# Kernel tuning notes

Measured on AMD Instinct MI355X. Metric: run time of the kernel, lower is better.

The kernel has to match this reference:

```python
import jax, jax.numpy as jnp
import numpy as np

B, C, W, H, HEADS = 32, 512, 32, 32, 8
D = C // HEADS
N = W * H
LN_EPS = 1e-5


def setup_inputs() -> dict:
    key = jax.random.key(0)
    ks = jax.random.split(key, 11)
    s = 1.0 / np.sqrt(C)
    return {
        "x": jax.random.normal(ks[0], (B, C, W, H), jnp.float32),
        "Wq": jax.random.normal(ks[1], (C, C), jnp.float32) * s,
        "bq": jax.random.normal(ks[2], (C,), jnp.float32) * 0.01,
        "Wk": jax.random.normal(ks[3], (C, C), jnp.float32) * s,
        "bk": jax.random.normal(ks[4], (C,), jnp.float32) * 0.01,
        "Wv": jax.random.normal(ks[5], (C, C), jnp.float32) * s,
        "bv": jax.random.normal(ks[6], (C,), jnp.float32) * 0.01,
        "rel_h": jax.random.normal(ks[7], (1, HEADS, D, 1, H), jnp.float32),
        "rel_w": jax.random.normal(ks[8], (1, HEADS, D, W, 1), jnp.float32),
        "ln_w": jnp.ones((C, W, H), jnp.float32),
        "ln_b": jnp.zeros((C, W, H), jnp.float32),
    }


def reference(x, Wq, bq, Wk, bk, Wv, bv, rel_h, rel_w, ln_w, ln_b):
    b, c, w, h = x.shape
    nh, d, n = HEADS, c // HEADS, w * h

    def proj(Wm, bm):
        # 1x1 conv == per-pixel linear: out[b,o,w,h] = sum_c Wm[o,c] x[b,c,w,h] + bm[o]
        y = jnp.einsum('bcwh,oc->bowh', x, Wm) + bm[None, :, None, None]
        return y.reshape(b, nh, d, n)

    q = proj(Wq, bq)  # [B,h,d,N]
    k = proj(Wk, bk)
    v = proj(Wv, bv)

    # content-content: q^T k -> [B,h,N,N]
    cc = jnp.einsum('bhdn,bhdm->bhnm', q, k)
    # content-position: (rel_h + rel_w) flattened to [h,d,N], permuted, matmul with q
    pos = (rel_h + rel_w).reshape(nh, d, n)  # [h,d,N]
    cp = jnp.einsum('hdn,bhdm->bhnm', pos, q)

    attn = jax.nn.softmax(cc + cp, axis=-1)  # [B,h,N,N]
    # out = v @ attn^T  -> [B,h,d,N]
    out = jnp.einsum('bhdn,bhmn->bhdm', v, attn)
    out = out.reshape(b, c, w, h)

    # LayerNorm over [C,W,H] with elementwise affine, then residual
    mu = jnp.mean(out, axis=(1, 2, 3), keepdims=True)
    var = jnp.var(out, axis=(1, 2, 3), keepdims=True)
    out = (out - mu) * jax.lax.rsqrt(var + LN_EPS) * ln_w[None] + ln_b[None]
    return out + x
```

## Files before the change

### kernel.cpp

```cpp
#include <hip/hip_runtime.h>
#include <stdint.h>

typedef _Float16 f16x8 __attribute__((ext_vector_type(8)));
typedef _Float16 f16x4 __attribute__((ext_vector_type(4)));
typedef __fp16   fp16x2 __attribute__((ext_vector_type(2)));
typedef float f32x4  __attribute__((ext_vector_type(4)));

__device__ __forceinline__ _Float16 f2h(float f){ return (_Float16)f; }

#define NB   32
#define NC   512
#define NH   8
#define ND   64
#define NN   1024

#define LOG2E 1.44269504f

__global__ __launch_bounds__(256) void wt_conv(const float* __restrict__ Wq,
                                               const float* __restrict__ Wk,
                                               const float* __restrict__ Wv,
                                               _Float16* __restrict__ Wt){
  int idx = blockIdx.x * 256 + threadIdx.x;
  int sel = idx >> 18;
  const float* W = (sel == 0) ? Wq : (sel == 1) ? Wk : Wv;
  Wt[idx] = f2h(W[idx & 262143]);
}

__global__ __launch_bounds__(256) void transpose_x(const float* __restrict__ x,
                                                   _Float16* __restrict__ xT){
  __shared__ float tile[32][33];
  int n0 = blockIdx.x * 32, c0 = blockIdx.y * 32, b = blockIdx.z;
  int t = threadIdx.x;
  int tn = t & 31, tc = t >> 5;
#pragma unroll
  for (int k = 0; k < 4; k++)
    tile[tc + 8*k][tn] = x[(b*NC + c0 + tc + 8*k)*NN + n0 + tn];
  __syncthreads();
#pragma unroll
  for (int k = 0; k < 4; k++)
    xT[(b*NN + n0 + tc + 8*k)*NC + c0 + tn] = f2h(tile[tn][tc + 8*k]);
}

__global__ __launch_bounds__(256) void pos_conv(const float* __restrict__ rel_h,
                                                const float* __restrict__ rel_w,
                                                _Float16* __restrict__ pos_t){
  int idx = blockIdx.x * 256 + threadIdx.x;
  int d = idx & 63, n = (idx >> 6) & 1023, h = idx >> 16;
  int ww = n >> 5, hh = n & 31;
  float v = rel_h[(h*ND + d)*32 + hh] + rel_w[(h*ND + d)*32 + ww];
  pos_t[idx] = f2h(v);
}

#define ASTR 72
#define TSTR 136

__global__ __launch_bounds__(256) void proj_gemm(const _Float16* __restrict__ Wt,
                                                 const _Float16* __restrict__ xT,
                                                 const float* __restrict__ bq,
                                                 const float* __restrict__ bk,
                                                 const float* __restrict__ bv,
                                                 _Float16* __restrict__ q_ws,
                                                 _Float16* __restrict__ k_ws,
                                                 _Float16* __restrict__ v_ws){
  __shared__ _Float16 smem[2 * 128 * ASTR];
  _Float16* As = smem;
  _Float16* Bs = smem + 128 * ASTR;

  int mt = blockIdx.x;
  int nt = blockIdx.y;
  int b  = blockIdx.z;
  int t = threadIdx.x, lane = t & 63, w = t >> 6;
  int wm = w >> 1, wn = w & 1;
  int lr = lane & 15, lg = lane >> 4;

  f32x4 acc[4][4];
#pragma unroll
  for (int i = 0; i < 4; i++)
#pragma unroll
    for (int j = 0; j < 4; j++) acc[i][j] = (f32x4)0.f;

  const _Float16* Arow = Wt + mt * 128 * NC;
  const _Float16* Brow = xT + (b * NN + nt * 128) * NC;

  for (int k0 = 0; k0 < NC; k0 += 64){
    __syncthreads();
#pragma unroll
    for (int i = 0; i < 4; i++){
      int lin = t + 256 * i;
      int row = lin >> 3, c8 = lin & 7;
      *(f16x8*)(As + row*ASTR + c8*8) = *(const f16x8*)(Arow + row*NC + k0 + c8*8);
      *(f16x8*)(Bs + row*ASTR + c8*8) = *(const f16x8*)(Brow + row*NC + k0 + c8*8);
    }
    __syncthreads();
#pragma unroll
    for (int ks = 0; ks < 2; ks++){
      f16x8 af[4], bfr[4];
#pragma unroll
      for (int mi = 0; mi < 4; mi++)
        af[mi] = *(f16x8*)(As + (wm*64 + mi*16 + lr)*ASTR + ks*32 + lg*8);
#pragma unroll
      for (int nj = 0; nj < 4; nj++)
        bfr[nj] = *(f16x8*)(Bs + (wn*64 + nj*16 + lr)*ASTR + ks*32 + lg*8);
#pragma unroll
      for (int mi = 0; mi < 4; mi++)
#pragma unroll
        for (int nj = 0; nj < 4; nj++)
          acc[mi][nj] = __builtin_amdgcn_mfma_f32_16x16x32_f16(af[mi], bfr[nj], acc[mi][nj], 0, 0, 0);
    }
  }
  __syncthreads();

  if (mt < 8){
    _Float16* Ts = smem;
#pragma unroll
    for (int mi = 0; mi < 4; mi++){
      int o0 = wm*64 + mi*16 + 4*lg;
      int og = mt*128 + o0;
      int sel = og >> 9, oo = og & 511;
      const float* bias = (sel == 0) ? bq : bk;
      float sc = (sel == 0) ? LOG2E : 1.f;
      float b0 = bias[oo], b1 = bias[oo+1], b2 = bias[oo+2], b3 = bias[oo+3];
#pragma unroll
      for (int nj = 0; nj < 4; nj++){
        int pix = wn*64 + nj*16 + lr;
        f16x4 pk;
        pk[0] = f2h((acc[mi][nj][0] + b0) * sc);
        pk[1] = f2h((acc[mi][nj][1] + b1) * sc);
        pk[2] = f2h((acc[mi][nj][2] + b2) * sc);
        pk[3] = f2h((acc[mi][nj][3] + b3) * sc);
        *(f16x4*)(Ts + pix*TSTR + o0) = pk;
      }
    }
    __syncthreads();
#pragma unroll
    for (int i = 0; i < 8; i++){
      int lin = t + 256 * i;
      int c_o = lin & 15, pix = lin >> 4;
      f16x8 v = *(f16x8*)(Ts + pix*TSTR + c_o*8);
      int og = mt*128 + c_o*8;
      int sel = og >> 9, oo = og & 511;
      int head = oo >> 6, d = oo & 63;
      _Float16* dst = (sel == 0) ? q_ws : k_ws;
      *(f16x8*)(dst + (((b*NH + head)*NN) + nt*128 + pix)*ND + d) = v;
    }
  } else {
    _Float16* Ts2 = smem;
#pragma unroll
    for (int mi = 0; mi < 4; mi++){
      int o0 = wm*64 + mi*16 + 4*lg;
      int vb = (mt - 8)*128 + o0;
      float b0 = bv[vb], b1 = bv[vb+1], b2 = bv[vb+2], b3 = bv[vb+3];
#pragma unroll
      for (int nj = 0; nj < 4; nj++){
        int pix = wn*64 + nj*16 + lr;
        Ts2[(o0+0)*TSTR + pix] = f2h(acc[mi][nj][0] + b0);
        Ts2[(o0+1)*TSTR + pix] = f2h(acc[mi][nj][1] + b1);
        Ts2[(o0+2)*TSTR + pix] = f2h(acc[mi][nj][2] + b2);
        Ts2[(o0+3)*TSTR + pix] = f2h(acc[mi][nj][3] + b3);
      }
    }
    __syncthreads();
#pragma unroll
    for (int i = 0; i < 8; i++){
      int lin = t + 256 * i;
      int pix8 = lin & 15, o_loc = lin >> 4;
      f16x8 v = *(f16x8*)(Ts2 + o_loc*TSTR + pix8*8);
      int vb = (mt - 8)*128 + o_loc;
      int head = vb >> 6, d = vb & 63;
      *(f16x8*)(v_ws + ((b*NH + head)*ND + d)*NN + nt*128 + pix8*8) = v;
    }
  }
}

#define KSTR 136
#define PSTR 72
#define OSTR 65
#define OFF_VT 8704
#define OFF_P  12800

__global__ __launch_bounds__(256, 3) void attn_kernel(const _Float16* __restrict__ q_ws,
                                                      const _Float16* __restrict__ k_ws,
                                                      const _Float16* __restrict__ v_ws,
                                                      const _Float16* __restrict__ pos_t,
                                                      float* __restrict__ out,
                                                      float* __restrict__ red){
  __shared__ _Float16 smem[22016];
  __shared__ float lnred[8];
  _Float16* Kc = smem;
  _Float16* Vt = smem + OFF_VT;
  _Float16* Pl = smem + OFF_P;

  int bid = blockIdx.x;
  int sid = (bid & 7) * 256 + (bid >> 3);
  int qt = sid & 7, h = (sid >> 3) & 7, b = sid >> 6;

  int t = threadIdx.x, lane = t & 63, w = t >> 6;
  int lr = lane & 15, lg = lane >> 4;

  const _Float16* qbh = q_ws + (b*NH + h) * NN * ND;
  const _Float16* kbh = k_ws + (b*NH + h) * NN * ND;
  const _Float16* vbh = v_ws + (b*NH + h) * ND * NN;
  const _Float16* pph = pos_t + h * NN * ND;

  f16x8 qreg[2][4];
#pragma unroll
  for (int qi = 0; qi < 2; qi++){
    int row = qt*128 + w*32 + qi*16 + lr;
#pragma unroll
    for (int ks = 0; ks < 4; ks++){
      const _Float16* src = (ks < 2) ? (qbh + row*ND + ks*32 + lg*8)
                                     : (pph + row*ND + (ks-2)*32 + lg*8);
      qreg[qi][ks] = *(const f16x8*)src;
    }
  }

  int k_row = t >> 4, k_c8 = t & 15;
  int v_d = t >> 3, v_ch = t & 7;

  f16x8 kst[4], vst[2];
#pragma unroll
  for (int i = 0; i < 4; i++){
    int row = k_row + i*16;
    const _Float16* src = (k_c8 < 8) ? (kbh + row*ND + k_c8*8)
                                     : (qbh + row*ND + (k_c8 - 8)*8);
    kst[i] = *(const f16x8*)src;
  }
#pragma unroll
  for (int i = 0; i < 2; i++)
    vst[i] = *(const f16x8*)(vbh + (v_d + i*32)*NN + v_ch*8);

  float m_r[2], l_r[2];
  f32x4 oacc[2][4];
#pragma unroll
  for (int qi = 0; qi < 2; qi++){ m_r[qi] = -1e30f; l_r[qi] = 0.f; }
#pragma unroll
  for (int qi = 0; qi < 2; qi++)
#pragma unroll
    for (int dj = 0; dj < 4; dj++) oacc[qi][dj] = (f32x4)0.f;

  for (int tt = 0; tt < 16; tt++){
    __syncthreads();
#pragma unroll
    for (int i = 0; i < 4; i++)
      *(f16x8*)(Kc + (k_row + i*16)*KSTR + k_c8*8) = kst[i];
#pragma unroll
    for (int i = 0; i < 2; i++){
      int d = v_d + i*32;
      *(f16x8*)(Vt + d*64 + ((v_ch*8) ^ ((d & 7) << 3))) = vst[i];
    }
    if (tt < 15){
      int n1 = tt*64 + 64;
#pragma unroll
      for (int i = 0; i < 4; i++){
        int row = n1 + k_row + i*16;
        const _Float16* src = (k_c8 < 8) ? (kbh + row*ND + k_c8*8)
                                         : (qbh + row*ND + (k_c8 - 8)*8);
        kst[i] = *(const f16x8*)src;
      }
#pragma unroll
      for (int i = 0; i < 2; i++)
        vst[i] = *(const f16x8*)(vbh + (v_d + i*32)*NN + n1 + v_ch*8);
    }
    __syncthreads();

    f32x4 sacc[4][2];
#pragma unroll
    for (int kt = 0; kt < 4; kt++)
#pragma unroll
      for (int qi = 0; qi < 2; qi++) sacc[kt][qi] = (f32x4)0.f;
#pragma unroll
    for (int ks = 0; ks < 4; ks++){
      f16x8 kf[4];
#pragma unroll
      for (int kt = 0; kt < 4; kt++)
        kf[kt] = *(f16x8*)(Kc + (kt*16 + lr)*KSTR + ks*32 + lg*8);
#pragma unroll
      for (int kt = 0; kt < 4; kt++)
#pragma unroll
        for (int qi = 0; qi < 2; qi++)
          sacc[kt][qi] = __builtin_amdgcn_mfma_f32_16x16x32_f16(kf[kt], qreg[qi][ks], sacc[kt][qi], 0, 0, 0);
    }

#pragma unroll
    for (int qi = 0; qi < 2; qi++){
      float m0 = fmaxf(fmaxf(sacc[0][qi][0], sacc[0][qi][1]), fmaxf(sacc[0][qi][2], sacc[0][qi][3]));
      float m1 = fmaxf(fmaxf(sacc[1][qi][0], sacc[1][qi][1]), fmaxf(sacc[1][qi][2], sacc[1][qi][3]));
      float m2 = fmaxf(fmaxf(sacc[2][qi][0], sacc[2][qi][1]), fmaxf(sacc[2][qi][2], sacc[2][qi][3]));
      float m3 = fmaxf(fmaxf(sacc[3][qi][0], sacc[3][qi][1]), fmaxf(sacc[3][qi][2], sacc[3][qi][3]));
      float mx = fmaxf(fmaxf(m0, m1), fmaxf(m2, m3));
      mx = fmaxf(mx, __shfl_xor(mx, 16));
      mx = fmaxf(mx, __shfl_xor(mx, 32));
      if (!__all(mx - m_r[qi] <= 11.f)){
        float mn = fmaxf(m_r[qi], mx);
        float cr = __builtin_exp2f(m_r[qi] - mn);
        m_r[qi] = mn;
        l_r[qi] *= cr;
#pragma unroll
        for (int r = 0; r < 4; r++){
          float crow = __shfl(cr, 4*lg + r);
#pragma unroll
          for (int dj = 0; dj < 4; dj++) oacc[qi][dj][r] *= crow;
        }
      }
      float mn = m_r[qi];
      float ts = 0.f;
#pragma unroll
      for (int kt = 0; kt < 4; kt++){
        float p0 = __builtin_exp2f(sacc[kt][qi][0] - mn);
        float p1 = __builtin_exp2f(sacc[kt][qi][1] - mn);
        float p2 = __builtin_exp2f(sacc[kt][qi][2] - mn);
        float p3 = __builtin_exp2f(sacc[kt][qi][3] - mn);
        ts += (p0 + p1) + (p2 + p3);
        union { fp16x2 h2[2]; uint2 u2; } pu;
        pu.h2[0] = __builtin_amdgcn_cvt_pkrtz(p0, p1);
        pu.h2[1] = __builtin_amdgcn_cvt_pkrtz(p2, p3);
        *(uint2*)(Pl + (w*32 + qi*16 + lr)*PSTR + kt*16 + lg*4) = pu.u2;
      }
      ts += __shfl_xor(ts, 16);
      ts += __shfl_xor(ts, 32);
      l_r[qi] += ts;
    }

#pragma unroll
    for (int ks = 0; ks < 2; ks++){
      f16x8 pf[2], vf[4];
#pragma unroll
      for (int qi = 0; qi < 2; qi++)
        pf[qi] = *(f16x8*)(Pl + (w*32 + qi*16 + lr)*PSTR + ks*32 + lg*8);
#pragma unroll
      for (int dj = 0; dj < 4; dj++){
        int row = dj*16 + lr;
        vf[dj] = *(f16x8*)(Vt + row*64 + ((ks*32 + lg*8) ^ ((row & 7) << 3)));
      }
#pragma unroll
      for (int qi = 0; qi < 2; qi++)
#pragma unroll
        for (int dj = 0; dj < 4; dj++)
          oacc[qi][dj] = __builtin_amdgcn_mfma_f32_16x16x32_f16(pf[qi], vf[dj], oacc[qi][dj], 0, 0, 0);
    }
  }

  float s_ln = 0.f, q_ln = 0.f;
  __syncthreads();
  float* Ot = (float*)smem;
#pragma unroll
  for (int p = 0; p < 2; p++){
    if ((w >> 1) == p){
      int wl = w & 1;
#pragma unroll
      for (int qi = 0; qi < 2; qi++){
        float iv = 1.f / l_r[qi];
#pragma unroll
        for (int r = 0; r < 4; r++){
          float invr = __shfl(iv, 4*lg + r);
#pragma unroll
          for (int dj = 0; dj < 4; dj++){
            float val = oacc[qi][dj][r] * invr;
            s_ln += val; q_ln += val*val;
            Ot[(wl*32 + qi*16 + 4*lg + r)*OSTR + dj*16 + lr] = val;
          }
        }
      }
    }
    __syncthreads();
#pragma unroll
    for (int i = 0; i < 4; i++){
      int lin = t + 256*i;
      int d = lin >> 4, jc = lin & 15;
      float4 v;
      v.x = Ot[(jc*4 + 0)*OSTR + d];
      v.y = Ot[(jc*4 + 1)*OSTR + d];
      v.z = Ot[(jc*4 + 2)*OSTR + d];
      v.w = Ot[(jc*4 + 3)*OSTR + d];
      *(float4*)(out + (b*NC + h*ND + d)*NN + qt*128 + p*64 + jc*4) = v;
    }
    __syncthreads();
  }

#pragma unroll
  for (int off = 1; off < 64; off <<= 1){
    s_ln += __shfl_xor(s_ln, off);
    q_ln += __shfl_xor(q_ln, off);
  }
  if (lane == 0){ lnred[w*2] = s_ln; lnred[w*2 + 1] = q_ln; }
  __syncthreads();
  if (t == 0){
    int idx = ((b*NH + h)*8 + qt)*2;
    red[idx]     = lnred[0] + lnred[2] + lnred[4] + lnred[6];
    red[idx + 1] = lnred[1] + lnred[3] + lnred[5] + lnred[7];
  }
}

__global__ void ln_stats(const float* __restrict__ red, float* __restrict__ stats){
  int b = threadIdx.x;
  if (b < 32){
    float s = 0.f, sq = 0.f;
    for (int j = 0; j < 64; j++){ s += red[(b*64 + j)*2]; sq += red[(b*64 + j)*2 + 1]; }
    float mu  = s * (1.f / 524288.f);
    float var = sq * (1.f / 524288.f) - mu*mu;
    stats[b*2] = mu;
    stats[b*2 + 1] = rsqrtf(var + 1e-5f);
  }
}

__global__ __launch_bounds__(256) void ln_apply(const float* __restrict__ x,
                                                const float* __restrict__ lw,
                                                const float* __restrict__ lb,
                                                const float* __restrict__ stats,
                                                float* __restrict__ out){
  int tid = blockIdx.x*256 + threadIdx.x;
  for (int i4 = tid; i4 < 4194304; i4 += 524288){
    int b = i4 >> 17;
    int r4 = i4 & 131071;
    float mu = stats[b*2], rs = stats[b*2 + 1];
    float4 o  = ((const float4*)out)[i4];
    float4 xv = ((const float4*)x)[i4];
    float4 ww = ((const float4*)lw)[r4];
    float4 bb = ((const float4*)lb)[r4];
    o.x = (o.x - mu)*rs*ww.x + bb.x + xv.x;
    o.y = (o.y - mu)*rs*ww.y + bb.y + xv.y;
    o.z = (o.z - mu)*rs*ww.z + bb.z + xv.z;
    o.w = (o.w - mu)*rs*ww.w + bb.w + xv.w;
    ((float4*)out)[i4] = o;
  }
}

extern "C" void kernel_launch(void* const* d_in, const int* in_sizes, int n_in,
                              void* d_out, int out_size, void* d_ws, size_t ws_size,
                              hipStream_t stream){
  (void)in_sizes; (void)n_in; (void)out_size; (void)ws_size;
  const float* x    = (const float*)d_in[0];
  const float* Wq   = (const float*)d_in[1];
  const float* bq   = (const float*)d_in[2];
  const float* Wk   = (const float*)d_in[3];
  const float* bk   = (const float*)d_in[4];
  const float* Wv   = (const float*)d_in[5];
  const float* bv   = (const float*)d_in[6];
  const float* relh = (const float*)d_in[7];
  const float* relw = (const float*)d_in[8];
  const float* lnw  = (const float*)d_in[9];
  const float* lnb  = (const float*)d_in[10];
  float* out = (float*)d_out;
  char* ws = (char*)d_ws;

  _Float16* q_ws  = (_Float16*)(ws);
  _Float16* k_ws  = (_Float16*)(ws + 33554432);
  _Float16* v_ws  = (_Float16*)(ws + 67108864);
  _Float16* xT    = (_Float16*)(ws + 100663296);
  _Float16* Wt    = (_Float16*)(ws + 134217728);
  _Float16* pos_t = (_Float16*)(ws + 135790592);
  float* red   = (float*)(ws + 136839168);
  float* stats = red + 4096;

  wt_conv    <<<3072, 256, 0, stream>>>(Wq, Wk, Wv, Wt);
  transpose_x<<<dim3(32, 16, 32), 256, 0, stream>>>(x, xT);
  pos_conv   <<<2048, 256, 0, stream>>>(relh, relw, pos_t);
  proj_gemm  <<<dim3(12, 8, 32), 256, 0, stream>>>(Wt, xT, bq, bk, bv, q_ws, k_ws, v_ws);
  attn_kernel<<<2048, 256, 0, stream>>>(q_ws, k_ws, v_ws, pos_t, out, red);
  ln_stats   <<<1, 64, 0, stream>>>(red, stats);
  ln_apply   <<<2048, 256, 0, stream>>>(x, lnw, lnb, stats, out);
}
```

Baseline: 334.0 us.

## Keep softmax probabilities in registers and transpose PV MFMA to drop LDS staging

```diff
diff --git a/kernel.cpp b/kernel.cpp
--- a/kernel.cpp
+++ b/kernel.cpp
@@ -173,22 +173,18 @@
 }
 
 #define KSTR 136
-#define PSTR 72
-#define OSTR 65
 #define OFF_VT 8704
-#define OFF_P  12800
-
-__global__ __launch_bounds__(256, 3) void attn_kernel(const _Float16* __restrict__ q_ws,
-                                                      const _Float16* __restrict__ k_ws,
-                                                      const _Float16* __restrict__ v_ws,
-                                                      const _Float16* __restrict__ pos_t,
-                                                      float* __restrict__ out,
-                                                      float* __restrict__ red){
-  __shared__ _Float16 smem[22016];
+
+__global__ __launch_bounds__(256) void attn_kernel(const _Float16* __restrict__ q_ws,
+                                                   const _Float16* __restrict__ k_ws,
+                                                   const _Float16* __restrict__ v_ws,
+                                                   const _Float16* __restrict__ pos_t,
+                                                   float* __restrict__ out,
+                                                   float* __restrict__ red){
+  __shared__ _Float16 smem[12800];
   __shared__ float lnred[8];
   _Float16* Kc = smem;
   _Float16* Vt = smem + OFF_VT;
-  _Float16* Pl = smem + OFF_P;
 
   int bid = blockIdx.x;
   int sid = (bid & 7) * 256 + (bid >> 3);
@@ -215,19 +211,7 @@
   }
 
   int k_row = t >> 4, k_c8 = t & 15;
-  int v_d = t >> 3, v_ch = t & 7;
-
-  f16x8 kst[4], vst[2];
-#pragma unroll
-  for (int i = 0; i < 4; i++){
-    int row = k_row + i*16;
-    const _Float16* src = (k_c8 < 8) ? (kbh + row*ND + k_c8*8)
-                                     : (qbh + row*ND + (k_c8 - 8)*8);
-    kst[i] = *(const f16x8*)src;
-  }
-#pragma unroll
-  for (int i = 0; i < 2; i++)
-    vst[i] = *(const f16x8*)(vbh + (v_d + i*32)*NN + v_ch*8);
+  int v_d0 = t >> 3, v_ch = t & 7;
 
   float m_r[2], l_r[2];
   f32x4 oacc[2][4];
@@ -238,28 +222,22 @@
 #pragma unroll
     for (int dj = 0; dj < 4; dj++) oacc[qi][dj] = (f32x4)0.f;
 
-  for (int tt = 0; tt < 16; tt++){
-    __syncthreads();
-#pragma unroll
-    for (int i = 0; i < 4; i++)
-      *(f16x8*)(Kc + (k_row + i*16)*KSTR + k_c8*8) = kst[i];
+  union pfu { fp16x2 h2[4]; f16x8 v8; };
+  union vfu { f16x4 v4[2]; f16x8 v8; };
+
+  for (int n0 = 0; n0 < NN; n0 += 64){
+    __syncthreads();
+#pragma unroll
+    for (int i = 0; i < 4; i++){
+      int row = k_row + i*16;
+      const _Float16* src = (k_c8 < 8) ? (kbh + (n0 + row)*ND + k_c8*8)
+                                       : (qbh + (n0 + row)*ND + (k_c8 - 8)*8);
+      *(f16x8*)(Kc + row*KSTR + k_c8*8) = *(const f16x8*)src;
+    }
 #pragma unroll
     for (int i = 0; i < 2; i++){
-      int d = v_d + i*32;
-      *(f16x8*)(Vt + d*64 + ((v_ch*8) ^ ((d & 7) << 3))) = vst[i];
-    }
-    if (tt < 15){
-      int n1 = tt*64 + 64;
-#pragma unroll
-      for (int i = 0; i < 4; i++){
-        int row = n1 + k_row + i*16;
-        const _Float16* src = (k_c8 < 8) ? (kbh + row*ND + k_c8*8)
-                                         : (qbh + row*ND + (k_c8 - 8)*8);
-        kst[i] = *(const f16x8*)src;
-      }
-#pragma unroll
-      for (int i = 0; i < 2; i++)
-        vst[i] = *(const f16x8*)(vbh + (v_d + i*32)*NN + n1 + v_ch*8);
+      int d = v_d0 + i*32;
+      *(f16x8*)(Vt + d*64 + ((v_ch*8) ^ ((d & 7) << 3))) = *(const f16x8*)(vbh + d*NN + n0 + v_ch*8);
     }
     __syncthreads();
 
@@ -281,6 +259,7 @@
           sacc[kt][qi] = __builtin_amdgcn_mfma_f32_16x16x32_f16(kf[kt], qreg[qi][ks], sacc[kt][qi], 0, 0, 0);
     }
 
+    pfu pa[2][2];
 #pragma unroll
     for (int qi = 0; qi < 2; qi++){
       float m0 = fmaxf(fmaxf(sacc[0][qi][0], sacc[0][qi][1]), fmaxf(sacc[0][qi][2], sacc[0][qi][3]));
@@ -291,16 +270,12 @@
       mx = fmaxf(mx, __shfl_xor(mx, 16));
       mx = fmaxf(mx, __shfl_xor(mx, 32));
       if (!__all(mx - m_r[qi] <= 11.f)){
-        float mn = fmaxf(m_r[qi], mx);
-        float cr = __builtin_exp2f(m_r[qi] - mn);
-        m_r[qi] = mn;
+        float mn2 = fmaxf(m_r[qi], mx);
+        float cr = __builtin_exp2f(m_r[qi] - mn2);
+        m_r[qi] = mn2;
         l_r[qi] *= cr;
 #pragma unroll
-        for (int r = 0; r < 4; r++){
-          float crow = __shfl(cr, 4*lg + r);
-#pragma unroll
-          for (int dj = 0; dj < 4; dj++) oacc[qi][dj][r] *= crow;
-        }
+        for (int dj = 0; dj < 4; dj++) oacc[qi][dj] *= cr;
       }
       float mn = m_r[qi];
       float ts = 0.f;
@@ -311,10 +286,8 @@
         float p2 = __builtin_exp2f(sacc[kt][qi][2] - mn);
         float p3 = __builtin_exp2f(sacc[kt][qi][3] - mn);
         ts += (p0 + p1) + (p2 + p3);
-        union { fp16x2 h2[2]; uint2 u2; } pu;
-        pu.h2[0] = __builtin_amdgcn_cvt_pkrtz(p0, p1);
-        pu.h2[1] = __builtin_amdgcn_cvt_pkrtz(p2, p3);
-        *(uint2*)(Pl + (w*32 + qi*16 + lr)*PSTR + kt*16 + lg*4) = pu.u2;
+        pa[qi][kt >> 1].h2[((kt & 1) << 1) + 0] = __builtin_amdgcn_cvt_pkrtz(p0, p1);
+        pa[qi][kt >> 1].h2[((kt & 1) << 1) + 1] = __builtin_amdgcn_cvt_pkrtz(p2, p3);
       }
       ts += __shfl_xor(ts, 16);
       ts += __shfl_xor(ts, 32);
@@ -323,58 +296,38 @@
 
 #pragma unroll
     for (int ks = 0; ks < 2; ks++){
-      f16x8 pf[2], vf[4];
-#pragma unroll
-      for (int qi = 0; qi < 2; qi++)
-        pf[qi] = *(f16x8*)(Pl + (w*32 + qi*16 + lr)*PSTR + ks*32 + lg*8);
+      f16x8 vf[4];
 #pragma unroll
       for (int dj = 0; dj < 4; dj++){
         int row = dj*16 + lr;
-        vf[dj] = *(f16x8*)(Vt + row*64 + ((ks*32 + lg*8) ^ ((row & 7) << 3)));
+        int sw = (row & 7) << 3;
+        vfu u;
+        u.v4[0] = *(f16x4*)(Vt + row*64 + ((ks*32 + lg*4) ^ sw));
+        u.v4[1] = *(f16x4*)(Vt + row*64 + ((ks*32 + 16 + lg*4) ^ sw));
+        vf[dj] = u.v8;
       }
 #pragma unroll
       for (int qi = 0; qi < 2; qi++)
 #pragma unroll
         for (int dj = 0; dj < 4; dj++)
-          oacc[qi][dj] = __builtin_amdgcn_mfma_f32_16x16x32_f16(pf[qi], vf[dj], oacc[qi][dj], 0, 0, 0);
+          oacc[qi][dj] = __builtin_amdgcn_mfma_f32_16x16x32_f16(vf[dj], pa[qi][ks].v8, oacc[qi][dj], 0, 0, 0);
     }
   }
 
   float s_ln = 0.f, q_ln = 0.f;
-  __syncthreads();
-  float* Ot = (float*)smem;
-#pragma unroll
-  for (int p = 0; p < 2; p++){
-    if ((w >> 1) == p){
-      int wl = w & 1;
-#pragma unroll
-      for (int qi = 0; qi < 2; qi++){
-        float iv = 1.f / l_r[qi];
-#pragma unroll
-        for (int r = 0; r < 4; r++){
-          float invr = __shfl(iv, 4*lg + r);
-#pragma unroll
-          for (int dj = 0; dj < 4; dj++){
-            float val = oacc[qi][dj][r] * invr;
-            s_ln += val; q_ln += val*val;
-            Ot[(wl*32 + qi*16 + 4*lg + r)*OSTR + dj*16 + lr] = val;
-          }
-        }
-      }
-    }
-    __syncthreads();
-#pragma unroll
-    for (int i = 0; i < 4; i++){
-      int lin = t + 256*i;
-      int d = lin >> 4, jc = lin & 15;
-      float4 v;
-      v.x = Ot[(jc*4 + 0)*OSTR + d];
-      v.y = Ot[(jc*4 + 1)*OSTR + d];
-      v.z = Ot[(jc*4 + 2)*OSTR + d];
-      v.w = Ot[(jc*4 + 3)*OSTR + d];
-      *(float4*)(out + (b*NC + h*ND + d)*NN + qt*128 + p*64 + jc*4) = v;
-    }
-    __syncthreads();
+#pragma unroll
+  for (int qi = 0; qi < 2; qi++){
+    float iv = 1.f / l_r[qi];
+    int qcol = qt*128 + w*32 + qi*16 + lr;
+#pragma unroll
+    for (int dj = 0; dj < 4; dj++){
+#pragma unroll
+      for (int r = 0; r < 4; r++){
+        float val = oacc[qi][dj][r] * iv;
+        s_ln += val; q_ln += val*val;
+        out[(b*NC + h*ND + dj*16 + 4*lg + r)*NN + qcol] = val;
+      }
+    }
   }
 
 #pragma unroll
```

Result: no change. 340.6 us (+2.0%).
